# Kernel tuning notes

Hardware: AMD Instinct MI355X
Metric: run time of the kernel (lower is better)

The kernel has to match this reference:

```python
import jax, jax.numpy as jnp
import numpy as np

N_NODES = 50000


def gcn_conv(x, edge_index, W, b, n_nodes):
    """GCNConv: out = D^-1/2 (A+I) D^-1/2 (x W) + b (symmetric normalization, self-loops)."""
    h = x @ W  # transform first (lower dim), like PyG GCNConv
    src, dst = edge_index[0], edge_index[1]
    loop = jnp.arange(n_nodes, dtype=src.dtype)
    src = jnp.concatenate([src, loop])
    dst = jnp.concatenate([dst, loop])
    ones = jnp.ones(src.shape[0], dtype=h.dtype)
    deg = jax.ops.segment_sum(ones, dst, num_segments=n_nodes)
    dinv = jnp.where(deg > 0, jax.lax.rsqrt(deg), 0.0)
    norm = dinv[src] * dinv[dst]  # [E+N]
    msg = h[src] * norm[:, None]  # gather + scale
    out = jax.ops.segment_sum(msg, dst, num_segments=n_nodes)  # scatter-add
    return out + b


def setup_inputs() -> dict:
    key = jax.random.key(0)
    ks = jax.random.split(key, 9)
    input_dim, latent_dim = 128, 32
    h1 = 2 * latent_dim  # 64
    x = jax.random.normal(ks[0], (N_NODES, input_dim), dtype=jnp.float32)
    edge_index = jax.random.randint(ks[1], (2, 800000), 0, N_NODES, dtype=jnp.int64)
    s1 = 1.0 / np.sqrt(input_dim)
    s2 = 1.0 / np.sqrt(h1)
    s3 = 1.0 / np.sqrt(latent_dim)
    W1 = jax.random.uniform(ks[2], (input_dim, h1), jnp.float32, -s1, s1)
    b1 = jax.random.uniform(ks[3], (h1,), jnp.float32, -s1, s1)
    W2 = jax.random.uniform(ks[4], (h1, latent_dim), jnp.float32, -s2, s2)
    b2 = jax.random.uniform(ks[5], (latent_dim,), jnp.float32, -s2, s2)
    Wl = jax.random.uniform(ks[6], (latent_dim, input_dim), jnp.float32, -s3, s3)
    bl = jax.random.uniform(ks[7], (input_dim,), jnp.float32, -s3, s3)
    return {"x": x, "edge_index": edge_index, "W1": W1, "b1": b1,
            "W2": W2, "b2": b2, "Wl": Wl, "bl": bl}


def reference(x, edge_index, W1, b1, W2, b2, Wl, bl):
    n = x.shape[0]
    h = gcn_conv(x, edge_index, W1, b1, n)
    h = jax.nn.relu(h)
    # dropout is identity in eval mode
    h = gcn_conv(h, edge_index, W2, b2, n)
    h = jax.nn.relu(h)
    return h @ Wl + bl
```

## Files before the change

kernel.cpp:

```cpp
#include <hip/hip_runtime.h>

#define F0 128
#define F1 64
#define F2 32
#define CAP 64

__device__ __forceinline__ int rfl(int v) { return __builtin_amdgcn_readfirstlane(v); }

__device__ __forceinline__ unsigned short f2b(float f) {
    unsigned u = __float_as_uint(f);
    return (unsigned short)((u + 0x7fffu + ((u >> 16) & 1u)) >> 16);
}
__device__ __forceinline__ float b2f(unsigned short u) {
    return __uint_as_float(((unsigned)u) << 16);
}

__device__ __forceinline__ void acc8(float* a, uint4 v) {
    a[0] += __uint_as_float(v.x << 16);
    a[1] += __uint_as_float(v.x & 0xffff0000u);
    a[2] += __uint_as_float(v.y << 16);
    a[3] += __uint_as_float(v.y & 0xffff0000u);
    a[4] += __uint_as_float(v.z << 16);
    a[5] += __uint_as_float(v.z & 0xffff0000u);
    a[6] += __uint_as_float(v.w << 16);
    a[7] += __uint_as_float(v.w & 0xffff0000u);
}

__global__ __launch_bounds__(256) void bucket1(const int* __restrict__ src,
                                               const int* __restrict__ dst,
                                               int* __restrict__ deg,
                                               int* __restrict__ buck, int E) {
    int e = blockIdx.x * 256 + threadIdx.x;
    if (e < E) {
        int d = dst[e];
        int pos = atomicAdd(&deg[d], 1);
        if (pos < CAP) buck[(d << 6) + pos] = src[e];
    }
}

__global__ __launch_bounds__(256) void gemm1(const float* __restrict__ x,
                                             const float* __restrict__ W1,
                                             const int* __restrict__ deg,
                                             unsigned short* __restrict__ xws1b,
                                             int N, int kb) {
    __shared__ float sx[64][132];
    __shared__ float sW[64][64];
    int tid = threadIdx.x;
    int row0 = blockIdx.x * 64;

    for (int i = tid; i < 2048; i += 256) {
        int r = i >> 5, kq = i & 31;
        int gr = row0 + r;
        float4 v = make_float4(0.f, 0.f, 0.f, 0.f);
        if (gr < N) v = ((const float4*)(x + (size_t)gr * F0))[kq];
        *(float4*)(&sx[r][kq << 2]) = v;
    }

    int tx = tid & 15, ty = tid >> 4;
    int c0 = tx * 4, r0 = ty * 4;
    float acc[4][4] = {};

    const float4* W4 = (const float4*)W1;
    float4* sW4 = (float4*)(&sW[0][0]);

    for (int p = 0; p < 2; ++p) {
        if (p) __syncthreads();
        for (int i = tid; i < 1024; i += 256) sW4[i] = W4[p * 1024 + i];
        __syncthreads();
        int kbase = p * 64;
        for (int k = 0; k < kb; k += 4) {
            float a[4][4], b[4][4];
            #pragma unroll
            for (int rr = 0; rr < 4; ++rr)
                *(float4*)&a[rr][0] = *(const float4*)&sx[r0 + rr][kbase + k];
            #pragma unroll
            for (int j = 0; j < 4; ++j)
                *(float4*)&b[j][0] = *(const float4*)&sW[k + j][c0];
            #pragma unroll
            for (int j = 0; j < 4; ++j)
                #pragma unroll
                for (int rr = 0; rr < 4; ++rr)
                    #pragma unroll
                    for (int cc = 0; cc < 4; ++cc)
                        acc[rr][cc] += a[rr][j] * b[j][cc];
        }
    }

    #pragma unroll
    for (int rr = 0; rr < 4; ++rr) {
        int gr = row0 + r0 + rr;
        if (gr < N) {
            float s = rsqrtf((float)(deg[gr] + 1));
            ushort4 o;
            o.x = f2b(acc[rr][0] * s); o.y = f2b(acc[rr][1] * s);
            o.z = f2b(acc[rr][2] * s); o.w = f2b(acc[rr][3] * s);
            *(ushort4*)&xws1b[gr * F1 + c0] = o;
        }
    }
}

__global__ __launch_bounds__(256, 5) void gather1f(const int* __restrict__ buck,
                                                   const int* __restrict__ deg,
                                                   const unsigned short* __restrict__ xb,
                                                   const float* __restrict__ b1,
                                                   const float* __restrict__ W2,
                                                   unsigned short* __restrict__ xws2b,
                                                   int N) {
    __shared__ float h1s[4][F1];
    int tid = threadIdx.x;
    int wv = tid >> 6, lane = tid & 63;
    int grp = lane >> 3;
    int fb = (lane & 7) << 3;
    int b3 = (lane >> 3) & 1, b4 = (lane >> 4) & 1, b5 = lane >> 5;
    int f = fb + b3 * 4 + b4 * 2 + b5;
    float breg = b1[f];
    int c = lane & 31, half = b5;
    int k0 = half * 32;
    float wreg[32];
    #pragma unroll
    for (int j = 0; j < 32; ++j) wreg[j] = W2[(k0 + j) * F2 + c];

    int stride = gridDim.x * 4;
    int node = blockIdx.x * 4 + wv;

    int cnt = 0;
    float dd = 0.f;
    bool p0 = false, p1 = false;
    uint4 v0, v1;
    if (node < N) {
        int cr = rfl(deg[node]);
        dd = rsqrtf((float)(cr + 1));
        cnt = cr < CAP ? cr : CAP;
        int start = node << 6;
        p0 = grp < cnt; p1 = grp + 8 < cnt;
        int s0 = 0, s1 = 0;
        if (p0) s0 = buck[start + grp];
        if (p1) s1 = buck[start + grp + 8];
        if (p0) v0 = *(const uint4*)(xb + (size_t)s0 * F1 + fb);
        if (p1) v1 = *(const uint4*)(xb + (size_t)s1 * F1 + fb);
    }

    while (node < N) {
        int start = node << 6;
        int nnode = node + stride;
        int ncnt = 0;
        float ndd = 0.f;
        bool np0 = false, np1 = false;
        uint4 nv0, nv1;
        if (nnode < N) {
            int ncr = rfl(deg[nnode]);
            ndd = rsqrtf((float)(ncr + 1));
            ncnt = ncr < CAP ? ncr : CAP;
            int nstart = nnode << 6;
            np0 = grp < ncnt; np1 = grp + 8 < ncnt;
            int ns0 = 0, ns1 = 0;
            if (np0) ns0 = buck[nstart + grp];
            if (np1) ns1 = buck[nstart + grp + 8];
            if (np0) nv0 = *(const uint4*)(xb + (size_t)ns0 * F1 + fb);
            if (np1) nv1 = *(const uint4*)(xb + (size_t)ns1 * F1 + fb);
        }
        bool p2 = (16 + grp) < cnt;
        uint4 v2;
        if (p2) {
            int s2 = buck[start + 16 + grp];
            v2 = *(const uint4*)(xb + (size_t)s2 * F1 + fb);
        }
        uint4 vs = *(const uint4*)(xb + (size_t)node * F1 + fb);

        float acc[8] = {};
        if (p0) acc8(acc, v0);
        if (p1) acc8(acc, v1);
        if (p2) acc8(acc, v2);
        for (int j = 24; j < cnt; j += 8) {
            int e = j + grp;
            if (e < cnt) {
                int s = buck[start + e];
                uint4 w = *(const uint4*)(xb + (size_t)s * F1 + fb);
                acc8(acc, w);
            }
        }
        if (grp == 0) acc8(acc, vs);

        float L[4];
        #pragma unroll
        for (int i = 0; i < 4; ++i) {
            float s = b3 ? acc[i] : acc[i + 4];
            float r = __shfl_xor(s, 8, 64);
            L[i] = (b3 ? acc[i + 4] : acc[i]) + r;
        }
        float M[2];
        #pragma unroll
        for (int i = 0; i < 2; ++i) {
            float s = b4 ? L[i] : L[i + 2];
            float r = __shfl_xor(s, 16, 64);
            M[i] = (b4 ? L[i + 2] : L[i]) + r;
        }
        float sx_ = b5 ? M[0] : M[1];
        float rx = __shfl_xor(sx_, 32, 64);
        float hv = (b5 ? M[1] : M[0]) + rx;

        hv = fmaxf(dd * hv + breg, 0.f);
        h1s[wv][f] = hv;

        float dot = 0.f;
        #pragma unroll
        for (int t = 0; t < 8; ++t) {
            float4 hb = *(const float4*)&h1s[wv][k0 + t * 4];
            dot += hb.x * wreg[t * 4] + hb.y * wreg[t * 4 + 1]
                 + hb.z * wreg[t * 4 + 2] + hb.w * wreg[t * 4 + 3];
        }
        dot += __shfl_xor(dot, 32, 64);
        if (half == 0) xws2b[node * F2 + c] = f2b(dot * dd);

        node = nnode; cnt = ncnt; dd = ndd;
        p0 = np0; p1 = np1; v0 = nv0; v1 = nv1;
    }
}

__global__ __launch_bounds__(256, 4) void gather2f(const int* __restrict__ buck,
                                                   const int* __restrict__ deg,
                                                   const unsigned short* __restrict__ xb,
                                                   const float* __restrict__ b2,
                                                   const float* __restrict__ Wl,
                                                   const float* __restrict__ bl,
                                                   float* __restrict__ out, int N) {
    __shared__ float h2s[4][F2];
    int tid = threadIdx.x;
    int wv = tid >> 6, lane = tid & 63;
    int grp = lane >> 2;
    int fb = (lane & 3) << 3;
    int bb2 = (lane >> 2) & 1, b3 = (lane >> 3) & 1, b4 = (lane >> 4) & 1, b5 = lane >> 5;
    int f = fb + bb2 * 4 + b3 * 2 + b4;
    float breg = b2[f];
    float blA = bl[lane], blB = bl[lane + 64];
    float wregA[32], wregB[32];
    #pragma unroll
    for (int j = 0; j < 32; ++j) {
        wregA[j] = Wl[j * F0 + lane];
        wregB[j] = Wl[j * F0 + lane + 64];
    }

    int stride = gridDim.x * 4;
    int node = blockIdx.x * 4 + wv;

    int cnt = 0;
    float dd = 0.f;
    bool p0 = false, p1 = false;
    uint4 v0, v1;
    if (node < N) {
        int cr = rfl(deg[node]);
        dd = rsqrtf((float)(cr + 1));
        cnt = cr < CAP ? cr : CAP;
        int start = node << 6;
        p0 = grp < cnt; p1 = grp + 16 < cnt;
        int s0 = 0, s1 = 0;
        if (p0) s0 = buck[start + grp];
        if (p1) s1 = buck[start + grp + 16];
        if (p0) v0 = *(const uint4*)(xb + (size_t)s0 * F2 + fb);
        if (p1) v1 = *(const uint4*)(xb + (size_t)s1 * F2 + fb);
    }

    while (node < N) {
        int start = node << 6;
        int nnode = node + stride;
        int ncnt = 0;
        float ndd = 0.f;
        bool np0 = false, np1 = false;
        uint4 nv0, nv1;
        if (nnode < N) {
            int ncr = rfl(deg[nnode]);
            ndd = rsqrtf((float)(ncr + 1));
            ncnt = ncr < CAP ? ncr : CAP;
            int nstart = nnode << 6;
            np0 = grp < ncnt; np1 = grp + 16 < ncnt;
            int ns0 = 0, ns1 = 0;
            if (np0) ns0 = buck[nstart + grp];
            if (np1) ns1 = buck[nstart + grp + 16];
            if (np0) nv0 = *(const uint4*)(xb + (size_t)ns0 * F2 + fb);
            if (np1) nv1 = *(const uint4*)(xb + (size_t)ns1 * F2 + fb);
        }
        uint4 vs = *(const uint4*)(xb + (size_t)node * F2 + fb);

        float acc[8] = {};
        if (p0) acc8(acc, v0);
        if (p1) acc8(acc, v1);
        for (int j = 32; j < cnt; j += 16) {
            int e = j + grp;
            if (e < cnt) {
                int s = buck[start + e];
                uint4 w = *(const uint4*)(xb + (size_t)s * F2 + fb);
                acc8(acc, w);
            }
        }
        if (grp == 0) acc8(acc, vs);

        float L[4];
        #pragma unroll
        for (int i = 0; i < 4; ++i) {
            float s = bb2 ? acc[i] : acc[i + 4];
            float r = __shfl_xor(s, 4, 64);
            L[i] = (bb2 ? acc[i + 4] : acc[i]) + r;
        }
        float M[2];
        #pragma unroll
        for (int i = 0; i < 2; ++i) {
            float s = b3 ? L[i] : L[i + 2];
            float r = __shfl_xor(s, 8, 64);
            M[i] = (b3 ? L[i + 2] : L[i]) + r;
        }
        float sx_ = b4 ? M[0] : M[1];
        float rx = __shfl_xor(sx_, 16, 64);
        float hv = (b4 ? M[1] : M[0]) + rx;
        hv += __shfl_xor(hv, 32, 64);

        hv = fmaxf(dd * hv + breg, 0.f);
        if (!b5) h2s[wv][f] = hv;

        float dA = 0.f, dB = 0.f;
        #pragma unroll
        for (int t = 0; t < 8; ++t) {
            float4 hb = *(const float4*)&h2s[wv][t * 4];
            dA += hb.x * wregA[t * 4] + hb.y * wregA[t * 4 + 1]
                + hb.z * wregA[t * 4 + 2] + hb.w * wregA[t * 4 + 3];
            dB += hb.x * wregB[t * 4] + hb.y * wregB[t * 4 + 1]
                + hb.z * wregB[t * 4 + 2] + hb.w * wregB[t * 4 + 3];
        }
        size_t ob = (size_t)node * F0;
        __builtin_nontemporal_store(dA + blA, &out[ob + lane]);
        __builtin_nontemporal_store(dB + blB, &out[ob + lane + 64]);

        node = nnode; cnt = ncnt; dd = ndd;
        p0 = np0; p1 = np1; v0 = nv0; v1 = nv1;
    }
}

extern "C" void kernel_launch(void* const* d_in, const int* in_sizes, int n_in,
                              void* d_out, int out_size, void* d_ws, size_t ws_size,
                              hipStream_t stream) {
    const float* x  = (const float*)d_in[0];
    const int*   ei = (const int*)d_in[1];
    const float* W1 = (const float*)d_in[2];
    const float* b1 = (const float*)d_in[3];
    const float* W2 = (const float*)d_in[4];
    const float* b2 = (const float*)d_in[5];
    const float* Wl = (const float*)d_in[6];
    const float* bl = (const float*)d_in[7];
    float* out = (float*)d_out;

    const int N = in_sizes[0] / F0;
    const int E = in_sizes[1] / 2;
    const int* src = ei;
    const int* dst = ei + E;

    char* ws = (char*)d_ws;
    size_t off = 0;
    auto alloc = [&](size_t bytes) {
        void* p = ws + off;
        off += (bytes + 255) & ~(size_t)255;
        return p;
    };
    int*            deg    = (int*)alloc((size_t)N * 4);
    int*            buck   = (int*)alloc((size_t)N * CAP * 4);
    unsigned short* xws1b  = (unsigned short*)alloc((size_t)N * F1 * 2);
    unsigned short* xws2b  = (unsigned short*)alloc((size_t)N * F2 * 2);

    hipMemsetAsync(deg, 0, (size_t)N * 4, stream);
    bucket1<<<(E + 255) / 256, 256, 0, stream>>>(src, dst, deg, buck, E);

    gemm1<<<(N + 63) / 64, 256, 0, stream>>>(x, W1, deg, xws1b, N, 64);
    gather1f<<<2048, 256, 0, stream>>>(buck, deg, xws1b, b1, W2, xws2b, N);
    gather2f<<<2048, 256, 0, stream>>>(buck, deg, xws2b, b2, Wl, bl, out, N);
}
```

Baseline: 210.4 us.

## Fuse edge bucketing into first GEMM and apply source normalization in gather

The separate bucket kernel is folded into gemm1: each thread buckets four edges using vectorized int4 loads before doing its GEMM tile, and the grid is sized to cover both the rows and the edges. Since degrees are no longer final when gemm1 writes its output, the source-side D^-1/2 scaling moves out of gemm1 and into gather1f, which reads deg[src] per neighbor and applies it with an FMA. This removes one kernel launch and lets edge bucketing overlap with GEMM work, but it adds a scattered deg read per gathered edge in gather1f.

Measured after the change: 208.4 us. No clear change (-1.0%).

```diff
diff --git a/kernel.cpp b/kernel.cpp
--- a/kernel.cpp
+++ b/kernel.cpp
@@ -26,27 +26,51 @@
     a[7] += __uint_as_float(v.w & 0xffff0000u);
 }
 
-__global__ __launch_bounds__(256) void bucket1(const int* __restrict__ src,
-                                               const int* __restrict__ dst,
-                                               int* __restrict__ deg,
-                                               int* __restrict__ buck, int E) {
-    int e = blockIdx.x * 256 + threadIdx.x;
-    if (e < E) {
-        int d = dst[e];
-        int pos = atomicAdd(&deg[d], 1);
-        if (pos < CAP) buck[(d << 6) + pos] = src[e];
-    }
+__device__ __forceinline__ void acc8s(float* a, uint4 v, float s) {
+    a[0] = fmaf(s, __uint_as_float(v.x << 16),          a[0]);
+    a[1] = fmaf(s, __uint_as_float(v.x & 0xffff0000u),  a[1]);
+    a[2] = fmaf(s, __uint_as_float(v.y << 16),          a[2]);
+    a[3] = fmaf(s, __uint_as_float(v.y & 0xffff0000u),  a[3]);
+    a[4] = fmaf(s, __uint_as_float(v.z << 16),          a[4]);
+    a[5] = fmaf(s, __uint_as_float(v.z & 0xffff0000u),  a[5]);
+    a[6] = fmaf(s, __uint_as_float(v.w << 16),          a[6]);
+    a[7] = fmaf(s, __uint_as_float(v.w & 0xffff0000u),  a[7]);
 }
 
 __global__ __launch_bounds__(256) void gemm1(const float* __restrict__ x,
                                              const float* __restrict__ W1,
-                                             const int* __restrict__ deg,
+                                             const int* __restrict__ src,
+                                             const int* __restrict__ dst,
+                                             int* __restrict__ deg,
+                                             int* __restrict__ buck,
                                              unsigned short* __restrict__ xws1b,
-                                             int N, int kb) {
+                                             int N, int E, int kb) {
     __shared__ float sx[64][132];
     __shared__ float sW[64][64];
     int tid = threadIdx.x;
     int row0 = blockIdx.x * 64;
+
+    {
+        int e0 = (blockIdx.x * 256 + tid) << 2;
+        if (e0 + 3 < E) {
+            int4 d4 = *(const int4*)(dst + e0);
+            int4 s4 = *(const int4*)(src + e0);
+            int p0 = atomicAdd(&deg[d4.x], 1);
+            int p1 = atomicAdd(&deg[d4.y], 1);
+            int p2 = atomicAdd(&deg[d4.z], 1);
+            int p3 = atomicAdd(&deg[d4.w], 1);
+            if (p0 < CAP) buck[(d4.x << 6) + p0] = s4.x;
+            if (p1 < CAP) buck[(d4.y << 6) + p1] = s4.y;
+            if (p2 < CAP) buck[(d4.z << 6) + p2] = s4.z;
+            if (p3 < CAP) buck[(d4.w << 6) + p3] = s4.w;
+        } else {
+            for (int e = e0; e < E; ++e) {
+                int d = dst[e];
+                int pos = atomicAdd(&deg[d], 1);
+                if (pos < CAP) buck[(d << 6) + pos] = src[e];
+            }
+        }
+    }
 
     for (int i = tid; i < 2048; i += 256) {
         int r = i >> 5, kq = i & 31;
@@ -90,10 +114,9 @@
     for (int rr = 0; rr < 4; ++rr) {
         int gr = row0 + r0 + rr;
         if (gr < N) {
-            float s = rsqrtf((float)(deg[gr] + 1));
             ushort4 o;
-            o.x = f2b(acc[rr][0] * s); o.y = f2b(acc[rr][1] * s);
-            o.z = f2b(acc[rr][2] * s); o.w = f2b(acc[rr][3] * s);
+            o.x = f2b(acc[rr][0]); o.y = f2b(acc[rr][1]);
+            o.z = f2b(acc[rr][2]); o.w = f2b(acc[rr][3]);
             *(ushort4*)&xws1b[gr * F1 + c0] = o;
         }
     }
@@ -126,6 +149,7 @@
     int cnt = 0;
     float dd = 0.f;
     bool p0 = false, p1 = false;
+    float sc0 = 0.f, sc1 = 0.f;
     uint4 v0, v1;
     if (node < N) {
         int cr = rfl(deg[node]);
@@ -136,8 +160,8 @@
         int s0 = 0, s1 = 0;
         if (p0) s0 = buck[start + grp];
         if (p1) s1 = buck[start + grp + 8];
-        if (p0) v0 = *(const uint4*)(xb + (size_t)s0 * F1 + fb);
-        if (p1) v1 = *(const uint4*)(xb + (size_t)s1 * F1 + fb);
+        if (p0) { sc0 = rsqrtf((float)(deg[s0] + 1)); v0 = *(const uint4*)(xb + (size_t)s0 * F1 + fb); }
+        if (p1) { sc1 = rsqrtf((float)(deg[s1] + 1)); v1 = *(const uint4*)(xb + (size_t)s1 * F1 + fb); }
     }
 
     while (node < N) {
@@ -146,6 +170,7 @@
         int ncnt = 0;
         float ndd = 0.f;
         bool np0 = false, np1 = false;
+        float nsc0 = 0.f, nsc1 = 0.f;
         uint4 nv0, nv1;
         if (nnode < N) {
             int ncr = rfl(deg[nnode]);
@@ -156,30 +181,33 @@
             int ns0 = 0, ns1 = 0;
             if (np0) ns0 = buck[nstart + grp];
             if (np1) ns1 = buck[nstart + grp + 8];
-            if (np0) nv0 = *(const uint4*)(xb + (size_t)ns0 * F1 + fb);
-            if (np1) nv1 = *(const uint4*)(xb + (size_t)ns1 * F1 + fb);
+            if (np0) { nsc0 = rsqrtf((float)(deg[ns0] + 1)); nv0 = *(const uint4*)(xb + (size_t)ns0 * F1 + fb); }
+            if (np1) { nsc1 = rsqrtf((float)(deg[ns1] + 1)); nv1 = *(const uint4*)(xb + (size_t)ns1 * F1 + fb); }
         }
         bool p2 = (16 + grp) < cnt;
+        float sc2 = 0.f;
         uint4 v2;
         if (p2) {
             int s2 = buck[start + 16 + grp];
+            sc2 = rsqrtf((float)(deg[s2] + 1));
             v2 = *(const uint4*)(xb + (size_t)s2 * F1 + fb);
         }
         uint4 vs = *(const uint4*)(xb + (size_t)node * F1 + fb);
 
         float acc[8] = {};
-        if (p0) acc8(acc, v0);
-        if (p1) acc8(acc, v1);
-        if (p2) acc8(acc, v2);
+        if (p0) acc8s(acc, v0, sc0);
+        if (p1) acc8s(acc, v1, sc1);
+        if (p2) acc8s(acc, v2, sc2);
         for (int j = 24; j < cnt; j += 8) {
             int e = j + grp;
             if (e < cnt) {
                 int s = buck[start + e];
+                float sc = rsqrtf((float)(deg[s] + 1));
                 uint4 w = *(const uint4*)(xb + (size_t)s * F1 + fb);
-                acc8(acc, w);
+                acc8s(acc, w, sc);
             }
         }
-        if (grp == 0) acc8(acc, vs);
+        if (grp == 0) acc8s(acc, vs, dd);
 
         float L[4];
         #pragma unroll
@@ -213,7 +241,7 @@
         if (half == 0) xws2b[node * F2 + c] = f2b(dot * dd);
 
         node = nnode; cnt = ncnt; dd = ndd;
-        p0 = np0; p1 = np1; v0 = nv0; v1 = nv1;
+        p0 = np0; p1 = np1; v0 = nv0; v1 = nv1; sc0 = nsc0; sc1 = nsc1;
     }
 }
 
@@ -365,9 +393,11 @@
     unsigned short* xws2b  = (unsigned short*)alloc((size_t)N * F2 * 2);
 
     hipMemsetAsync(deg, 0, (size_t)N * 4, stream);
-    bucket1<<<(E + 255) / 256, 256, 0, stream>>>(src, dst, deg, buck, E);
-
-    gemm1<<<(N + 63) / 64, 256, 0, stream>>>(x, W1, deg, xws1b, N, 64);
+
+    int gb_gemm = (N + 63) / 64;
+    int gb_edge = (E + 1023) / 1024;
+    int gb = gb_gemm > gb_edge ? gb_gemm : gb_edge;
+    gemm1<<<gb, 256, 0, stream>>>(x, W1, src, dst, deg, buck, xws1b, N, E, 64);
     gather1f<<<2048, 256, 0, stream>>>(buck, deg, xws1b, b1, W2, xws2b, N);
     gather2f<<<2048, 256, 0, stream>>>(buck, deg, xws2b, b2, Wl, bl, out, N);
 }
```
